# Performance work log

Measured on AMD Instinct MI355X. Metric: run time of the kernel, lower is better.

The kernel has to match this reference:

```python
import jax, jax.numpy as jnp
import numpy as np

B, LAT, H, K = 8, 128, 1024, 294
N, E = 100000, 1600000
XSIZE = 128.0
TAU = 0.5
STEPS = 3


def setup_inputs() -> dict:
    key = jax.random.key(0)
    ks = jax.random.split(key, 20)
    s_in = 1.0 / np.sqrt(LAT)
    s_h = 1.0 / np.sqrt(H)
    inp = {
        "latent": jax.random.normal(ks[0], (B, LAT), jnp.float32),
        "W0": jax.random.normal(ks[1], (LAT, H), jnp.float32) * s_in,
        "b0": jnp.zeros((H,), jnp.float32),
        "W1": jax.random.normal(ks[2], (H, H), jnp.float32) * s_h,
        "b1": jnp.zeros((H,), jnp.float32),
        "W2": jax.random.normal(ks[3], (H, H), jnp.float32) * s_h,
        "b2": jnp.zeros((H,), jnp.float32),
        "W3": jax.random.normal(ks[4], (H, H), jnp.float32) * s_h,
        "b3": jnp.zeros((H,), jnp.float32),
        # coefficient heads use normal(1e-4) init in the source
        "Wx": jax.random.normal(ks[5], (H, K), jnp.float32) * 1e-4,
        "bx": jnp.zeros((K,), jnp.float32),
        "Wy": jax.random.normal(ks[6], (H, K), jnp.float32) * 1e-4,
        "by": jnp.zeros((K,), jnp.float32),
        "Wz": jax.random.normal(ks[7], (H, K), jnp.float32) * 1e-4,
        "bz": jnp.zeros((K,), jnp.float32),
        # precomputed Zernike/spherical basis evaluated at the N coords: [K, N]
        "Z": jax.random.normal(ks[8], (K, N), jnp.float32),
        "edge_weights": jax.random.uniform(ks[9], (E,), jnp.float32),
        "edge_index": jax.random.randint(ks[10], (2, E), 0, N, jnp.int64),
    }
    return inp


def _decode_coefficients(latent, W0, b0, W1, b1, W2, b2, W3, b3,
                         Wx, bx, Wy, by, Wz, bz):
    h = jax.nn.relu(latent @ W0 + b0)
    for W, b in ((W1, b1), (W2, b2), (W3, b3)):
        h = jax.nn.relu(h + h @ W + b)  # residual MLP block
    return h @ Wx + bx, h @ Wy + by, h @ Wz + bz  # [B, K] each


def _diffuse(flow, edge_index, edge_weights):
    """Graph diffusion smoothing of per-node vectors. flow: [B, N, 3]."""
    src, dst = edge_index[0], edge_index[1]
    deg = jax.ops.segment_sum(edge_weights, dst, num_segments=N)
    deg = jnp.maximum(deg, 1e-6)[:, None, None]  # [N,1,1]
    f = jnp.transpose(flow, (1, 0, 2))  # [N, B, 3]
    w = edge_weights[:, None, None]
    for _ in range(STEPS):
        msg = f[src] * w                                        # gather  [E,B,3]
        agg = jax.ops.segment_sum(msg, dst, num_segments=N)     # scatter [N,B,3]
        f = (1.0 - TAU) * f + TAU * agg / deg
    return jnp.transpose(f, (1, 0, 2))  # [B, N, 3]


def reference(latent, W0, b0, W1, b1, W2, b2, W3, b3,
              Wx, bx, Wy, by, Wz, bz, Z, edge_weights, edge_index):
    cx, cy, cz = _decode_coefficients(latent, W0, b0, W1, b1, W2, b2, W3, b3,
                                      Wx, bx, Wy, by, Wz, bz)
    # basis evaluation: per-axis coefficients contracted with Zernike basis
    dx = jnp.einsum("bk,kn->bn", cx, Z)
    dy = jnp.einsum("bk,kn->bn", cy, Z)
    dz = jnp.einsum("bk,kn->bn", cz, Z)
    flow = (0.5 * XSIZE) * jnp.stack([dx, dy, dz], axis=-1)  # [B, N, 3]
    flow = _diffuse(flow, edge_index, edge_weights)
    reg = 1e-4 * jnp.sqrt(jnp.sum(cx ** 2 + cy ** 2 + cz ** 2))
    return flow, reg
```

## Files before the change

kernel.cpp:

```cpp
#include <hip/hip_runtime.h>
#include <math.h>

#define BB 8
#define LAT 128
#define HH 1024
#define KK 294
#define NN 100000
#define EE 1600000
#define NSTEPS 3
#define XS_HALF 64.0f

#define NB 391
#define CS 8
#define COB 28
#define COB2 30
#define EPT 8
#define EST 200000
#define EBLK 782
#define QA 196
#define GON 40

#define F3NB 391
#define KPAD 320

__constant__ float ccoefT[KPAD * 24];


__device__ __forceinline__ void mlp_part_body(int bid, const float* __restrict__ hin,
                                              const float* __restrict__ W,
                                              float* __restrict__ part, int jdim) {
    int it = bid & 15;
    int bs = bid >> 4;
    int tx = threadIdx.x;
    int il = tx & 63;
    int jg = tx >> 6;
    int i = it * 64 + il;
    int j0 = bs * 64;

    __shared__ float hs[8 * 64];
    for (int u = tx; u < 512; u += 256) {
        int b = u >> 6, lj = u & 63;
        hs[u] = hin[b * jdim + j0 + lj];
    }
    __syncthreads();

    float acc[8];
#pragma unroll
    for (int b = 0; b < 8; ++b) acc[b] = 0.0f;
#pragma unroll
    for (int jj = 0; jj < 16; ++jj) {
        int lj = jg * 16 + jj;
        float w = W[(size_t)(j0 + lj) * HH + i];
#pragma unroll
        for (int b = 0; b < 8; ++b) acc[b] += hs[b * 64 + lj] * w;
    }

    __shared__ float red[4][8][64];
#pragma unroll
    for (int b = 0; b < 8; ++b) red[jg][b][il] = acc[b];
    __syncthreads();
    for (int u = tx; u < 512; u += 256) {
        int b = u >> 6, ii = u & 63;
        float s = red[0][b][ii] + red[1][b][ii] + red[2][b][ii] + red[3][b][ii];
        part[(size_t)bs * 8192 + b * HH + it * 64 + ii] = s;
    }
}

__device__ __forceinline__ void mlp_comb_body(int bid, const float* __restrict__ part,
                                              int nsplit, const float* __restrict__ resid,
                                              const float* __restrict__ bias,
                                              float* __restrict__ hout) {
    int idx = bid * 256 + threadIdx.x;
    if (idx >= BB * HH) return;
    int i = idx & (HH - 1);
    float s = bias[i];
    if (resid) s += resid[idx];
    for (int bs = 0; bs < nsplit; ++bs) s += part[(size_t)bs * 8192 + idx];
    hout[idx] = fmaxf(s, 0.0f);
}

__device__ __forceinline__ void count_body(int gbid, const int* __restrict__ ei,
                                           int* __restrict__ cnt, int* __restrict__ rank) {
    int gid = gbid * 256 + threadIdx.x;
    if (gid >= EST) return;
    int d[EPT];
#pragma unroll
    for (int j = 0; j < EPT; ++j) d[j] = ei[EE + gid + j * EST];
#pragma unroll
    for (int j = 0; j < EPT; ++j) {
        int p = atomicAdd(&cnt[d[j]], 1);
        rank[gid + j * EST] = p;
    }
}

__device__ __forceinline__ void bsum_body(int bid, const int* __restrict__ cnt,
                                          int* __restrict__ bsum) {
    __shared__ int red[256];
    int i = bid * 256 + threadIdx.x;
    red[threadIdx.x] = (i < NN) ? cnt[i] : 0;
    __syncthreads();
    for (int off = 128; off > 0; off >>= 1) {
        if ((int)threadIdx.x < off) red[threadIdx.x] += red[threadIdx.x + off];
        __syncthreads();
    }
    if (threadIdx.x == 0) bsum[bid] = red[0];
}

__device__ __forceinline__ void bscan_body(const int* __restrict__ bsum,
                                           int* __restrict__ bpre,
                                           int* __restrict__ offs) {
    __shared__ int A[512], Bf[512];
    int t = threadIdx.x;
    A[t] = (t < NB) ? bsum[t] : 0;
    A[t + 256] = (t + 256 < NB) ? bsum[t + 256] : 0;
    __syncthreads();
    int* s = A;
    int* d = Bf;
    for (int off = 1; off < 512; off <<= 1) {
        d[t] = s[t] + ((t >= off) ? s[t - off] : 0);
        int u = t + 256;
        d[u] = s[u] + ((u >= off) ? s[u - off] : 0);
        __syncthreads();
        int* tmp = s; s = d; d = tmp;
    }
    if (t < NB) bpre[t] = (t == 0) ? 0 : s[t - 1];
    int u = t + 256;
    if (u < NB) bpre[u] = s[u - 1];
    if (t == 0) offs[NN] = s[NB - 1];
}

__device__ __forceinline__ void offs_body(int bid, const int* __restrict__ cnt,
                                          const int* __restrict__ bpre,
                                          int* __restrict__ offs) {
    __shared__ int part[256];
    int t = threadIdx.x;
    int i = bid * 256 + t;
    int v = (i < NN) ? cnt[i] : 0;
    part[t] = v;
    __syncthreads();
    for (int off = 1; off < 256; off <<= 1) {
        int u = (t >= off) ? part[t - off] : 0;
        __syncthreads();
        part[t] += u;
        __syncthreads();
    }
    if (i < NN) offs[i] = bpre[bid] + part[t] - v;
}

__device__ __forceinline__ void fill_body(int bid, const int* __restrict__ ei,
                                          const float* __restrict__ ew,
                                          const int* __restrict__ offs,
                                          const int* __restrict__ rank,
                                          int2* __restrict__ csr) {
    int gid = bid * 256 + threadIdx.x;
    if (gid >= EST) return;
    int s[EPT], d[EPT], r[EPT];
    float w[EPT];
#pragma unroll
    for (int j = 0; j < EPT; ++j) {
        int e = gid + j * EST;
        s[j] = ei[e];
        d[j] = ei[EE + e];
        w[j] = ew[e];
        r[j] = rank[e];
    }
#pragma unroll
    for (int j = 0; j < EPT; ++j) {
        int p = offs[d[j]] + r[j];
        int2 v;
        v.x = s[j];
        v.y = __float_as_int(w[j]);
        csr[p] = v;
    }
}

__device__ __forceinline__ void flow3_body(int bid, const float* __restrict__ Z,
                                           float* __restrict__ fout) {
    __shared__ float zl[4][4][8][64];

    int t = threadIdx.x;
    int lane = t & 63;
    int wu = __builtin_amdgcn_readfirstlane(t >> 6);

    int n = bid * 256 + (wu << 6) + lane;
    int nn = (n < NN) ? n : (NN - 1);
    const float* zn = Z + nn;

    float acc[24];
#pragma unroll
    for (int j = 0; j < 24; ++j) acc[j] = 0.0f;

    auto issue = [&](int cp) {
        int b = cp & 3;
#pragma unroll
        for (int d = 0; d < 8; ++d) {
            int r = cp * 8 + d;
            int rz = (r < KK) ? r : (KK - 1);
            __builtin_amdgcn_global_load_lds(
                (__attribute__((address_space(1))) unsigned int*)(zn + (size_t)rz * NN),
                (__attribute__((address_space(3))) unsigned int*)(&zl[wu][b][d][0]),
                4, 0, 0);
        }
    };

    issue(0); issue(1); issue(2);

#pragma unroll 1
    for (int c = 0; c < 37; ++c) {
        issue(c + 3);
        asm volatile("s_waitcnt vmcnt(24)" ::: "memory");
        __builtin_amdgcn_sched_barrier(0);
        int b = c & 3;
#pragma unroll
        for (int d = 0; d < 8; ++d) {
            float z = zl[wu][b][d][lane];
            const float* cf = &ccoefT[(c * 8 + d) * 24];
#pragma unroll
            for (int j = 0; j < 24; ++j) acc[j] = fmaf(cf[j], z, acc[j]);
        }
    }

    if (n < NN) {
        float buf4[24];
#pragma unroll
        for (int j = 0; j < 24; ++j) buf4[j] = XS_HALF * acc[j];
        float4* fr = (float4*)(fout + (size_t)n * 24);
#pragma unroll
        for (int q = 0; q < 6; ++q) fr[q] = ((const float4*)buf4)[q];
    }
}

__device__ __forceinline__ void reg_body(const float* __restrict__ coef,
                                         float* __restrict__ out_reg) {
    __shared__ float red[256];
    float s = 0.0f;
    for (int i = threadIdx.x; i < 3 * BB * KK; i += 256) {
        float v = coef[i];
        s += v * v;
    }
    red[threadIdx.x] = s;
    __syncthreads();
    for (int off = 128; off > 0; off >>= 1) {
        if ((int)threadIdx.x < off) red[threadIdx.x] += red[threadIdx.x + off];
        __syncthreads();
    }
    if (threadIdx.x == 0) out_reg[0] = 1e-4f * sqrtf(red[0]);
}


__global__ void K1_mlp0_cnt(const float* __restrict__ latent, const float* __restrict__ W0,
                            float* __restrict__ part, const int* __restrict__ ei,
                            int* __restrict__ cnt, int* __restrict__ rank) {
    if (blockIdx.x < 32) mlp_part_body(blockIdx.x, latent, W0, part, LAT);
    else count_body(blockIdx.x - 32, ei, cnt, rank);
}

__global__ void K2_comb0_cnt(const float* __restrict__ part, const float* __restrict__ b0,
                             float* __restrict__ hout, const int* __restrict__ ei,
                             int* __restrict__ cnt, int* __restrict__ rank) {
    if (blockIdx.x < 32) mlp_comb_body(blockIdx.x, part, 2, nullptr, b0, hout);
    else count_body(blockIdx.x - 32 + QA, ei, cnt, rank);
}

__global__ void K3_mlp1_cnt(const float* __restrict__ hin, const float* __restrict__ W1,
                            float* __restrict__ part, const int* __restrict__ ei,
                            int* __restrict__ cnt, int* __restrict__ rank) {
    if (blockIdx.x < 256) mlp_part_body(blockIdx.x, hin, W1, part, HH);
    else count_body(blockIdx.x - 256 + 2 * QA, ei, cnt, rank);
}

__global__ void K4_comb1_cnt(const float* __restrict__ part, const float* __restrict__ resid,
                             const float* __restrict__ b1, float* __restrict__ hout,
                             const int* __restrict__ ei, int* __restrict__ cnt,
                             int* __restrict__ rank) {
    if (blockIdx.x < 32) mlp_comb_body(blockIdx.x, part, 16, resid, b1, hout);
    else count_body(blockIdx.x - 32 + 3 * QA, ei, cnt, rank);
}

__global__ void K5_mlp2_bsum(const float* __restrict__ hin, const float* __restrict__ W2,
                             float* __restrict__ part, const int* __restrict__ cnt,
                             int* __restrict__ bsum) {
    if (blockIdx.x < 256) mlp_part_body(blockIdx.x, hin, W2, part, HH);
    else bsum_body(blockIdx.x - 256, cnt, bsum);
}

__global__ void K6_comb2_bscan(const float* __restrict__ part, const float* __restrict__ resid,
                               const float* __restrict__ b2, float* __restrict__ hout,
                               const int* __restrict__ bsum, int* __restrict__ bpre,
                               int* __restrict__ offs) {
    if (blockIdx.x < 32) mlp_comb_body(blockIdx.x, part, 16, resid, b2, hout);
    else bscan_body(bsum, bpre, offs);
}

__global__ void K7_mlp3_offs(const float* __restrict__ hin, const float* __restrict__ W3,
                             float* __restrict__ part, const int* __restrict__ cnt,
                             const int* __restrict__ bpre, int* __restrict__ offs) {
    if (blockIdx.x < 256) mlp_part_body(blockIdx.x, hin, W3, part, HH);
    else offs_body(blockIdx.x - 256, cnt, bpre, offs);
}

__global__ void K8_comb3(const float* __restrict__ part, const float* __restrict__ resid,
                         const float* __restrict__ b3, float* __restrict__ hout) {
    mlp_comb_body(blockIdx.x, part, 16, resid, b3, hout);
}

__global__ void k_coef_part(const float* __restrict__ h,
                            const float* __restrict__ Wx,
                            const float* __restrict__ Wy,
                            const float* __restrict__ Wz,
                            float* __restrict__ cpart) {
    int s = blockIdx.x / COB;
    int blk = blockIdx.x % COB;
    int o = blk * 256 + threadIdx.x;
    if (o >= 3 * BB * KK) return;
    int t = o / (BB * KK);
    int r = o % (BB * KK);
    int b = r / KK, k = r % KK;
    const float* W = (t == 0) ? Wx : ((t == 1) ? Wy : Wz);
    const float* hr = h + b * HH;
    int j0 = s * 128;
    float acc = 0.0f;
#pragma unroll 8
    for (int j = 0; j < 128; ++j) acc += hr[j0 + j] * W[(size_t)(j0 + j) * KK + k];
    cpart[(size_t)s * 7056 + o] = acc;
}

__global__ void k_coef_comb(const float* __restrict__ cpart,
                            const float* __restrict__ bx,
                            const float* __restrict__ by,
                            const float* __restrict__ bz,
                            float* __restrict__ coefT) {
    int o = blockIdx.x * 256 + threadIdx.x;
    if (o >= KPAD * 24) return;
    if (o >= 3 * BB * KK) {
        coefT[o] = 0.0f;
        return;
    }
    int t = o / (BB * KK);
    int r = o % (BB * KK);
    int b = r / KK;
    int k = r % KK;
    float s = ((t == 0) ? bx : ((t == 1) ? by : bz))[k];
#pragma unroll
    for (int i = 0; i < CS; ++i) s += cpart[(size_t)i * 7056 + o];
    coefT[k * 24 + b * 3 + t] = s;
}

__global__ void K_flow_fill_reg(const float* __restrict__ Z, float* __restrict__ fout,
                                const int* __restrict__ ei, const float* __restrict__ ew,
                                const int* __restrict__ offs, const int* __restrict__ rank,
                                int2* __restrict__ csr, const float* __restrict__ coefT,
                                float* __restrict__ out_reg) {
    if (blockIdx.x < F3NB) flow3_body(blockIdx.x, Z, fout);
    else if (blockIdx.x < F3NB + EBLK) fill_body(blockIdx.x - F3NB, ei, ew, offs, rank, csr);
    else reg_body(coefT, out_reg);
}

__global__ void k_gather(const int* __restrict__ offs, const int2* __restrict__ csr,
                         const float* __restrict__ fin, float* __restrict__ fout) {
    int idx = blockIdx.x * 256 + threadIdx.x;
    if (idx >= NN * 6) return;
    int n = idx / 6;
    int q = idx - n * 6;
    int beg = offs[n], end = offs[n + 1];
    const float4* f4 = (const float4*)fin;
    float4 acc = make_float4(0.f, 0.f, 0.f, 0.f);
    float wsum = 0.0f;
    int i = beg;
    for (; i + 4 <= end; i += 4) {
        int2 e[4];
#pragma unroll
        for (int u = 0; u < 4; ++u) e[u] = csr[i + u];
        float4 v[4];
#pragma unroll
        for (int u = 0; u < 4; ++u) v[u] = f4[(size_t)e[u].x * 6 + q];
#pragma unroll
        for (int u = 0; u < 4; ++u) {
            float w = __int_as_float(e[u].y);
            wsum += w;
            acc.x += w * v[u].x;
            acc.y += w * v[u].y;
            acc.z += w * v[u].z;
            acc.w += w * v[u].w;
        }
    }
    for (; i < end; ++i) {
        int2 e = csr[i];
        float w = __int_as_float(e.y);
        float4 fv = f4[(size_t)e.x * 6 + q];
        wsum += w;
        acc.x += w * fv.x;
        acc.y += w * fv.y;
        acc.z += w * fv.z;
        acc.w += w * fv.w;
    }
    float inv = 0.5f / fmaxf(wsum, 1e-6f);
    float4 fo = f4[(size_t)n * 6 + q];
    float4 r;
    r.x = 0.5f * fo.x + inv * acc.x;
    r.y = 0.5f * fo.y + inv * acc.y;
    r.z = 0.5f * fo.z + inv * acc.z;
    r.w = 0.5f * fo.w + inv * acc.w;
    ((float4*)fout)[(size_t)n * 6 + q] = r;
}

__global__ void k_gather_out(const int* __restrict__ offs, const int2* __restrict__ csr,
                             const float* __restrict__ fin, float* __restrict__ out) {
    __shared__ float ls[GON * 24];
    int t = threadIdx.x;
    int n0 = blockIdx.x * GON;
    if (t < GON * 6) {
        int ln = t / 6, q = t - 6 * ln;
        int n = n0 + ln;
        if (n < NN) {
            int beg = offs[n], end = offs[n + 1];
            const float4* f4 = (const float4*)fin;
            float4 acc = make_float4(0.f, 0.f, 0.f, 0.f);
            float wsum = 0.0f;
            int i = beg;
            for (; i + 4 <= end; i += 4) {
                int2 e[4];
#pragma unroll
                for (int u = 0; u < 4; ++u) e[u] = csr[i + u];
                float4 v[4];
#pragma unroll
                for (int u = 0; u < 4; ++u) v[u] = f4[(size_t)e[u].x * 6 + q];
#pragma unroll
                for (int u = 0; u < 4; ++u) {
                    float w = __int_as_float(e[u].y);
                    wsum += w;
                    acc.x += w * v[u].x;
                    acc.y += w * v[u].y;
                    acc.z += w * v[u].z;
                    acc.w += w * v[u].w;
                }
            }
            for (; i < end; ++i) {
                int2 e = csr[i];
                float w = __int_as_float(e.y);
                float4 fv = f4[(size_t)e.x * 6 + q];
                wsum += w;
                acc.x += w * fv.x;
                acc.y += w * fv.y;
                acc.z += w * fv.z;
                acc.w += w * fv.w;
            }
            float inv = 0.5f / fmaxf(wsum, 1e-6f);
            float4 fo = f4[(size_t)n * 6 + q];
            float* d = &ls[ln * 24 + q * 4];
            d[0] = 0.5f * fo.x + inv * acc.x;
            d[1] = 0.5f * fo.y + inv * acc.y;
            d[2] = 0.5f * fo.z + inv * acc.z;
            d[3] = 0.5f * fo.w + inv * acc.w;
        }
    }
    __syncthreads();
    int cnt = NN - n0; if (cnt > GON) cnt = GON;
    int per_b = cnt * 3;
    for (int b = 0; b < BB; ++b) {
        for (int u = t; u < per_b; u += 256) {
            int n = u / 3;
            int c = u - 3 * n;
            out[(size_t)b * (NN * 3) + (size_t)n0 * 3 + u] = ls[n * 24 + b * 3 + c];
        }
    }
}

extern "C" void kernel_launch(void* const* d_in, const int* in_sizes, int n_in,
                              void* d_out, int out_size, void* d_ws, size_t ws_size,
                              hipStream_t stream) {
    const float* latent = (const float*)d_in[0];
    const float* W0 = (const float*)d_in[1];
    const float* b0 = (const float*)d_in[2];
    const float* W1 = (const float*)d_in[3];
    const float* b1 = (const float*)d_in[4];
    const float* W2 = (const float*)d_in[5];
    const float* b2 = (const float*)d_in[6];
    const float* W3 = (const float*)d_in[7];
    const float* b3 = (const float*)d_in[8];
    const float* Wx = (const float*)d_in[9];
    const float* bx = (const float*)d_in[10];
    const float* Wy = (const float*)d_in[11];
    const float* by = (const float*)d_in[12];
    const float* Wz = (const float*)d_in[13];
    const float* bz = (const float*)d_in[14];
    const float* Z  = (const float*)d_in[15];
    const float* ew = (const float*)d_in[16];
    const int*   ei = (const int*)d_in[17];
    float* out = (float*)d_out;

    float* p = (float*)d_ws;
    float* h_a     = p; p += 8192;
    float* h_b     = p; p += 8192;
    float* hp      = p; p += 16 * 8192;
    float* coef    = p; p += KPAD * 24;
    float* cpart   = p; p += CS * 7056;
    int*   cnt     = (int*)p; p += 100000;
    int*   offs    = (int*)p; p += 100016;
    int*   bsum    = (int*)p; p += 512;
    int*   bpre    = (int*)p; p += 512;
    int*   rank    = (int*)p; p += 1600000;
    int2*  csr     = (int2*)p; p += 2 * 1600000;
    float* fpart   = p; p += (size_t)2 * NN * 24;

    hipMemsetAsync(cnt, 0, NN * sizeof(int), stream);

    K1_mlp0_cnt<<<32 + QA, 256, 0, stream>>>(latent, W0, hp, ei, cnt, rank);
    K2_comb0_cnt<<<32 + QA, 256, 0, stream>>>(hp, b0, h_a, ei, cnt, rank);
    K3_mlp1_cnt<<<256 + QA, 256, 0, stream>>>(h_a, W1, hp, ei, cnt, rank);
    K4_comb1_cnt<<<32 + (EBLK - 3 * QA), 256, 0, stream>>>(hp, h_a, b1, h_b, ei, cnt, rank);
    K5_mlp2_bsum<<<256 + NB, 256, 0, stream>>>(h_b, W2, hp, cnt, bsum);
    K6_comb2_bscan<<<32 + 1, 256, 0, stream>>>(hp, h_b, b2, h_a, bsum, bpre, offs);
    K7_mlp3_offs<<<256 + NB, 256, 0, stream>>>(h_a, W3, hp, cnt, bpre, offs);
    K8_comb3<<<32, 256, 0, stream>>>(hp, h_a, b3, h_b);
    k_coef_part<<<COB * CS, 256, 0, stream>>>(h_b, Wx, Wy, Wz, cpart);
    k_coef_comb<<<COB2, 256, 0, stream>>>(cpart, bx, by, bz, coef);
    hipMemcpyToSymbolAsync(HIP_SYMBOL(ccoefT), coef, KPAD * 24 * sizeof(float), 0,
                           hipMemcpyDeviceToDevice, stream);

    float* f0 = fpart;
    float* f1 = fpart + (size_t)NN * 24;
    K_flow_fill_reg<<<F3NB + EBLK + 1, 256, 0, stream>>>(Z, f0, ei, ew, offs, rank, csr,
                                                         coef, out + (size_t)BB * NN * 3);

    k_gather<<<(NN * 6 + 255) / 256, 256, 0, stream>>>(offs, csr, f0, f1);
    k_gather<<<(NN * 6 + 255) / 256, 256, 0, stream>>>(offs, csr, f1, f0);
    k_gather_out<<<(NN + GON - 1) / GON, 256, 0, stream>>>(offs, csr, f0, out);
}
```

Baseline: 486.8 us.

## Split basis contraction over K across two waves with LDS reduction

The flow basis kernel now assigns 128 nodes per block and splits the 294-term K reduction into two halves handled by paired waves, which combine partial sums through shared memory before writing. This doubles the number of blocks and halves the serial loop length per wave, aiming for more parallelism and latency hiding in the Z streaming contraction. It adds a shared-memory reduction with two block barriers. Padding constants shrink to match the new split.

```diff
diff --git a/kernel.cpp b/kernel.cpp
--- a/kernel.cpp
+++ b/kernel.cpp
@@ -13,15 +13,15 @@
 #define NB 391
 #define CS 8
 #define COB 28
-#define COB2 30
+#define COB2 29
 #define EPT 8
 #define EST 200000
 #define EBLK 782
 #define QA 196
 #define GON 40
 
-#define F3NB 391
-#define KPAD 320
+#define F4NB 782
+#define KPAD 304
 
 __constant__ float ccoefT[KPAD * 24];
 
@@ -174,16 +174,20 @@
     }
 }
 
-__device__ __forceinline__ void flow3_body(int bid, const float* __restrict__ Z,
+__device__ __forceinline__ void flow4_body(int bid, const float* __restrict__ Z,
                                            float* __restrict__ fout) {
     __shared__ float zl[4][4][8][64];
 
     int t = threadIdx.x;
     int lane = t & 63;
     int wu = __builtin_amdgcn_readfirstlane(t >> 6);
-
-    int n = bid * 256 + (wu << 6) + lane;
-    int nn = (n < NN) ? n : (NN - 1);
+    int pu = wu >> 1;
+    int hu = wu & 1;
+    int rbase = hu * 152;
+
+    int np = bid * 128 + pu * 64 + lane;
+    bool valid = np < NN;
+    int nn = valid ? np : (NN - 1);
     const float* zn = Z + nn;
 
     float acc[24];
@@ -194,7 +198,7 @@
         int b = cp & 3;
 #pragma unroll
         for (int d = 0; d < 8; ++d) {
-            int r = cp * 8 + d;
+            int r = rbase + cp * 8 + d;
             int rz = (r < KK) ? r : (KK - 1);
             __builtin_amdgcn_global_load_lds(
                 (__attribute__((address_space(1))) unsigned int*)(zn + (size_t)rz * NN),
@@ -206,7 +210,7 @@
     issue(0); issue(1); issue(2);
 
 #pragma unroll 1
-    for (int c = 0; c < 37; ++c) {
+    for (int c = 0; c < 19; ++c) {
         issue(c + 3);
         asm volatile("s_waitcnt vmcnt(24)" ::: "memory");
         __builtin_amdgcn_sched_barrier(0);
@@ -214,19 +218,36 @@
 #pragma unroll
         for (int d = 0; d < 8; ++d) {
             float z = zl[wu][b][d][lane];
-            const float* cf = &ccoefT[(c * 8 + d) * 24];
+            const float* cf = &ccoefT[(rbase + c * 8 + d) * 24];
 #pragma unroll
             for (int j = 0; j < 24; ++j) acc[j] = fmaf(cf[j], z, acc[j]);
         }
     }
 
-    if (n < NN) {
-        float buf4[24];
-#pragma unroll
-        for (int j = 0; j < 24; ++j) buf4[j] = XS_HALF * acc[j];
-        float4* fr = (float4*)(fout + (size_t)n * 24);
-#pragma unroll
-        for (int q = 0; q < 6; ++q) fr[q] = ((const float4*)buf4)[q];
+    asm volatile("s_waitcnt vmcnt(0)" ::: "memory");
+    __syncthreads();
+    float* red = (float*)zl + pu * 4096;
+    if (hu == 1) {
+        float4* r4 = (float4*)red;
+#pragma unroll
+        for (int j4 = 0; j4 < 6; ++j4)
+            r4[j4 * 64 + lane] = make_float4(acc[j4 * 4 + 0], acc[j4 * 4 + 1],
+                                             acc[j4 * 4 + 2], acc[j4 * 4 + 3]);
+    }
+    __syncthreads();
+    if (hu == 0 && valid) {
+        const float4* r4 = (const float4*)red;
+        float4* fr = (float4*)(fout + (size_t)np * 24);
+#pragma unroll
+        for (int j4 = 0; j4 < 6; ++j4) {
+            float4 v = r4[j4 * 64 + lane];
+            float4 o;
+            o.x = XS_HALF * (acc[j4 * 4 + 0] + v.x);
+            o.y = XS_HALF * (acc[j4 * 4 + 1] + v.y);
+            o.z = XS_HALF * (acc[j4 * 4 + 2] + v.z);
+            o.w = XS_HALF * (acc[j4 * 4 + 3] + v.w);
+            fr[j4] = o;
+        }
     }
 }
 
@@ -351,8 +372,8 @@
                                 const int* __restrict__ offs, const int* __restrict__ rank,
                                 int2* __restrict__ csr, const float* __restrict__ coefT,
                                 float* __restrict__ out_reg) {
-    if (blockIdx.x < F3NB) flow3_body(blockIdx.x, Z, fout);
-    else if (blockIdx.x < F3NB + EBLK) fill_body(blockIdx.x - F3NB, ei, ew, offs, rank, csr);
+    if (blockIdx.x < F4NB) flow4_body(blockIdx.x, Z, fout);
+    else if (blockIdx.x < F4NB + EBLK) fill_body(blockIdx.x - F4NB, ei, ew, offs, rank, csr);
     else reg_body(coefT, out_reg);
 }
 
@@ -520,7 +541,7 @@
 
     float* f0 = fpart;
     float* f1 = fpart + (size_t)NN * 24;
-    K_flow_fill_reg<<<F3NB + EBLK + 1, 256, 0, stream>>>(Z, f0, ei, ew, offs, rank, csr,
+    K_flow_fill_reg<<<F4NB + EBLK + 1, 256, 0, stream>>>(Z, f0, ei, ew, offs, rank, csr,
                                                          coef, out + (size_t)BB * NN * 3);
 
     k_gather<<<(NN * 6 + 255) / 256, 256, 0, stream>>>(offs, csr, f0, f1);
```

After: 495.3 us. No clear change (+1.7%).
